# Optimization experiments

Measured on AMD Instinct MI355X. Metric: run time of the kernel, lower is better.

The kernel has to match this reference:

```python
import jax, jax.numpy as jnp
import numpy as np

N_E = 100000       # entities
N_R = 1000         # relations
N_CLASSES = 20000  # class_index.max() + 1
E = 1000000        # edges (triples)
E_HIDDEN = 256
C_HIDDEN = 128
R_HIDDEN = 128
NEG_SLOPE = 0.01   # F.leaky_relu default


def leaky_relu(x):
    return jnp.where(x >= 0, x, NEG_SLOPE * x)


def segment_softmax(x, idx, num_segments):
    # torch_geometric-style scatter softmax over segments given by idx
    m = jax.ops.segment_max(x, idx, num_segments=num_segments)
    ex = jnp.exp(x - m[idx])
    s = jax.ops.segment_sum(ex, idx, num_segments=num_segments)
    return ex / (s[idx] + 1e-16)


def setup_inputs() -> dict:
    key = jax.random.key(0)
    ks = jax.random.split(key, 20)
    inv_c = 1.0 / np.sqrt(C_HIDDEN)
    inv_r = 1.0 / np.sqrt(R_HIDDEN)
    inv_e = 1.0 / np.sqrt(E_HIDDEN)
    inp = {
        "x_e": jax.random.normal(ks[0], (N_E, E_HIDDEN), jnp.float32),
        "edge_index": jax.random.randint(ks[1], (2, E), 0, N_E),
        "rel": jax.random.randint(ks[2], (E,), 0, N_R),
        "triple_num": jax.random.randint(ks[3], (E,), 0, N_E),
        "r_emb": jax.random.normal(ks[4], (N_R, R_HIDDEN), jnp.float32),
        "class_index": jax.random.randint(ks[5], (E,), 0, N_CLASSES),
        "head_class": jax.random.randint(ks[6], (N_CLASSES,), 0, N_E),
        # attention projection vectors (Linear(c_hidden,1,bias=False) weights)
        "a_h1": jax.random.normal(ks[7], (C_HIDDEN,), jnp.float32) * inv_c,
        "a_h2": jax.random.normal(ks[8], (C_HIDDEN,), jnp.float32) * inv_c,
        "a_h3": jax.random.normal(ks[9], (C_HIDDEN,), jnp.float32) * inv_c,
        "a_h4": jax.random.normal(ks[10], (C_HIDDEN,), jnp.float32) * inv_c,
        "a_t1": jax.random.normal(ks[11], (C_HIDDEN,), jnp.float32) * inv_c,
        "a_t2": jax.random.normal(ks[12], (C_HIDDEN,), jnp.float32) * inv_c,
        "a_t3": jax.random.normal(ks[13], (C_HIDDEN,), jnp.float32) * inv_c,
        "a_r1": jax.random.normal(ks[14], (R_HIDDEN,), jnp.float32) * inv_r,
        "a_r2": jax.random.normal(ks[15], (R_HIDDEN,), jnp.float32) * inv_r,
        "a_c": jax.random.normal(ks[16], (C_HIDDEN,), jnp.float32) * inv_c,
        # entity->class-space projections [e_hidden, c_hidden]
        "w_h": jax.random.normal(ks[17], (E_HIDDEN, C_HIDDEN), jnp.float32) * inv_e,
        "w_t": jax.random.normal(ks[18], (E_HIDDEN, C_HIDDEN), jnp.float32) * inv_e,
        # highway gate Linear(c_hidden, c_hidden)
        "hw_w": jax.random.normal(ks[19], (C_HIDDEN, C_HIDDEN), jnp.float32) * inv_c,
        "hw_b": jnp.zeros((C_HIDDEN,), jnp.float32),
    }
    return inp


def reference(x_e, edge_index, rel, triple_num, r_emb, class_index, head_class,
              a_h1, a_h2, a_h3, a_h4, a_t1, a_t2, a_t3, a_r1, a_r2, a_c,
              w_h, w_t, hw_w, hw_b):
    h_idx = edge_index[0]
    t_idx = edge_index[1]

    x_r_h = jax.nn.relu(x_e @ w_h)   # [N_e, C]
    x_r_t = jax.nn.relu(x_e @ w_t)   # [N_e, C]

    # --- level 1: edge attention over triple_num segments ---
    e1 = ((x_r_h @ a_h1)[h_idx] + (x_r_t @ a_t1)[t_idx]) / 2 + (r_emb @ a_r1)[rel]
    alpha = segment_softmax(leaky_relu(e1), triple_num, N_E)       # [E]

    x_t = x_r_t[t_idx] * alpha[:, None]                            # [E, C]
    norm = jnp.linalg.norm(x_t, axis=1, keepdims=True)
    x_t = x_t / jnp.maximum(norm, 1e-12)                           # F.normalize p=2

    # --- level 2: relation/class attention over class_index segments ---
    e_t = x_t @ a_t2                                               # [E]
    e_h = (x_r_h @ a_h2)[h_idx]
    e_r = (r_emb @ a_r2)[rel]
    e_r = (e_r + ((x_r_h @ a_h3)[h_idx] + (x_t @ a_t3)) / 2) / 2
    beta = segment_softmax(leaky_relu(e_t + e_r + e_h), class_index, N_CLASSES)

    # spmm: A[class_index[i], t_idx[i]] = beta[i];  x_class = A @ x_t
    x_class = jax.ops.segment_sum(beta[:, None] * x_t[t_idx],
                                  class_index, num_segments=N_CLASSES)  # [N_CLASSES, C]

    # --- level 3: class->head-entity attention over head_class segments ---
    e_c = (x_class @ a_c) + (x_r_h @ a_h4)[head_class]             # [N_CLASSES]
    gama = segment_softmax(leaky_relu(e_c), head_class, N_E)
    x_e_h = jax.ops.segment_sum(gama[:, None] * x_class,
                                head_class, num_segments=N_E)      # [N_e, C]

    # highway combine
    gate = jax.nn.sigmoid(x_r_h @ hw_w + hw_b)
    return gate * x_e_h + (1.0 - gate) * x_r_h
```

## Files before the change

kernel.cpp:

```cpp
#include <hip/hip_runtime.h>
#include <hip/hip_bf16.h>

#define LRELU(x) ((x) >= 0.f ? (x) : 0.01f * (x))

typedef __attribute__((ext_vector_type(8))) short short8v;
typedef __attribute__((ext_vector_type(4))) float f32x4;

__device__ inline unsigned fenc(float x) {
    unsigned u = __float_as_uint(x);
    return (u & 0x80000000u) ? ~u : (u | 0x80000000u);
}
__device__ inline float fdec(unsigned e) {
    return __uint_as_float((e & 0x80000000u) ? (e ^ 0x80000000u) : ~e);
}

__device__ inline float wred(float v) {
#pragma unroll
    for (int o = 32; o > 0; o >>= 1) v += __shfl_xor(v, o, 64);
    return v;
}
__device__ inline float wredmax(float v) {
#pragma unroll
    for (int o = 32; o > 0; o >>= 1) v = fmaxf(v, __shfl_xor(v, o, 64));
    return v;
}

__device__ inline unsigned short f2bu(float x) {
    __hip_bfloat16 b = __float2bfloat16(x);
    return *reinterpret_cast<unsigned short*>(&b);
}
__device__ inline float bu2f(unsigned short u) {
    return __uint_as_float((unsigned)u << 16);
}

__device__ inline f32x4 mfma16(short8v a, short8v b, f32x4 c) {
    return __builtin_amdgcn_mfma_f32_16x16x32_bf16(a, b, c, 0, 0, 0);
}

__device__ inline void gload16(const void* g, void* l) {
    __builtin_amdgcn_global_load_lds(
        (const __attribute__((address_space(1))) void*)g,
        (__attribute__((address_space(3))) void*)l, 16, 0, 0);
}

__global__ __launch_bounds__(256) void k_convW(
    const float* __restrict__ wh, const float* __restrict__ wt,
    const float* __restrict__ hww, unsigned short* __restrict__ wtb_hi,
    unsigned short* __restrict__ hwt_hi) {
    int id = blockIdx.x * 256 + threadIdx.x;
    if (id < 256 * 256) {
        int n = id >> 8, k = id & 255;
        float v = (n < 128) ? wh[(size_t)k * 128 + n] : wt[(size_t)k * 128 + (n - 128)];
        wtb_hi[(size_t)n * 256 + k] = f2bu(v);
    } else {
        int id2 = id - 256 * 256;
        if (id2 < 128 * 128) {
            int n = id2 >> 7, k = id2 & 127;
            hwt_hi[(size_t)n * 128 + k] = f2bu(hww[(size_t)k * 128 + n]);
        }
    }
}

__global__ __launch_bounds__(256) void k_rel(const float* __restrict__ remb,
                                             const float* __restrict__ ar2,
                                             float* __restrict__ er2, int NR) {
    int lane = threadIdx.x & 63;
    int r = blockIdx.x * 4 + (threadIdx.x >> 6);
    if (r >= NR) return;
    float v0 = remb[(size_t)r * 128 + lane];
    float v1 = remb[(size_t)r * 128 + 64 + lane];
    float p2 = wred(v0 * ar2[lane] + v1 * ar2[64 + lane]);
    if (lane == 0) er2[r] = p2;
}

template <int EPI>
__device__ __forceinline__ void mm_body(
    const float* __restrict__ Af32, const unsigned short* __restrict__ Ah,
    const unsigned short* __restrict__ Bh,
    unsigned short* __restrict__ oh0, unsigned short* __restrict__ oh1,
    float* __restrict__ o0, const float* __restrict__ bias,
    const float* __restrict__ xeh, int M,
    const float* __restrict__ ah2, const float* __restrict__ ah3,
    const float* __restrict__ ah4, const float* __restrict__ at2,
    const float* __restrict__ at3,
    float* __restrict__ hb, float* __restrict__ eh4o,
    float2* __restrict__ pta, const int* __restrict__ tidxg) {
    constexpr int KD = (EPI == 0) ? 256 : 128;
    constexpr int NSTEP = KD / 32;
    __shared__ unsigned short As_h[2][128 * 32];
    __shared__ unsigned short Bs_h[2][128 * 32];

    int bx = blockIdx.x;
    int half = (EPI == 0) ? (bx & 1) : 0;
    int mblk = (EPI == 0) ? (bx >> 1) : bx;
    int row0 = mblk * 128;
    if (row0 + 128 > M) row0 = M - 128;
    int tid = threadIdx.x, w = tid >> 6, l = tid & 63;
    int lr = l & 15, hi4 = l >> 4;
    int srow = l >> 2, sslot = l & 3;

    int arow0 = tid >> 2, aslot0 = tid & 3;
    int arow1 = (256 + tid) >> 2, aslot1 = tid & 3;
    int agr0 = (aslot0 ^ ((arow0 >> 1) & 3)) * 8;
    int agr1 = (aslot1 ^ ((arow1 >> 1) & 3)) * 8;
    float4 rA[4];

    f32x4 acc[2][8];
#pragma unroll
    for (int i = 0; i < 2; i++)
#pragma unroll
        for (int j = 0; j < 8; j++) acc[i][j] = (f32x4){0.f, 0.f, 0.f, 0.f};

    auto loadA = [&](int s) {
        int k0 = s * 32;
        const float* p0 = Af32 + (size_t)(row0 + arow0) * KD + k0 + agr0;
        const float* p1 = Af32 + (size_t)(row0 + arow1) * KD + k0 + agr1;
        rA[0] = *(const float4*)p0;
        rA[1] = *(const float4*)(p0 + 4);
        rA[2] = *(const float4*)p1;
        rA[3] = *(const float4*)(p1 + 4);
    };
    auto writeA = [&](int b) {
        short8v v0, v1;
        float x0[8] = {rA[0].x, rA[0].y, rA[0].z, rA[0].w,
                       rA[1].x, rA[1].y, rA[1].z, rA[1].w};
        float x1[8] = {rA[2].x, rA[2].y, rA[2].z, rA[2].w,
                       rA[3].x, rA[3].y, rA[3].z, rA[3].w};
#pragma unroll
        for (int j = 0; j < 8; j++) {
            v0[j] = (short)f2bu(x0[j]);
            v1[j] = (short)f2bu(x1[j]);
        }
        *(short8v*)&As_h[b][arow0 * 32 + aslot0 * 8] = v0;
        *(short8v*)&As_h[b][arow1 * 32 + aslot1 * 8] = v1;
    };
    auto stageB = [&](int s, int b) {
        int k0 = s * 32;
        constexpr int NU = (EPI == 0) ? 2 : 4;
#pragma unroll
        for (int i = 0; i < NU; i++) {
            int u = w * NU + i;
            int arr = u >> 3, ld = u & 7;
            int row = ld * 16 + srow;
            int klog = (sslot ^ ((row >> 1) & 3)) * 8;
            const unsigned short* src;
            unsigned short* dst;
            if constexpr (EPI == 0) {
                src = Bh + (size_t)(half * 128 + row) * KD;
                dst = Bs_h[b];
            } else {
                if (arr == 0) { src = Ah + (size_t)(row0 + row) * KD; dst = As_h[b]; }
                else          { src = Bh + (size_t)row * KD;          dst = Bs_h[b]; }
            }
            gload16(src + k0 + klog, dst + ld * 512);
        }
    };

    if constexpr (EPI == 0) {
        loadA(0);
        stageB(0, 0);
        writeA(0);
    } else {
        stageB(0, 0);
    }
    __syncthreads();
    for (int s = 0; s < NSTEP; s++) {
        int b = s & 1;
        if (s + 1 < NSTEP) {
            if constexpr (EPI == 0) loadA(s + 1);
            stageB(s + 1, b ^ 1);
        }

        short8v am_h[2];
#pragma unroll
        for (int mr = 0; mr < 2; mr++) {
            int r = w * 32 + mr * 16 + lr;
            int ko = (hi4 ^ ((r >> 1) & 3)) * 8;
            am_h[mr] = *(const short8v*)&As_h[b][r * 32 + ko];
        }
#pragma unroll
        for (int ncc = 0; ncc < 8; ncc += 4) {
            short8v bn_h[4];
#pragma unroll
            for (int j = 0; j < 4; j++) {
                int n = (ncc + j) * 16 + lr;
                int ko = (hi4 ^ ((n >> 1) & 3)) * 8;
                bn_h[j] = *(const short8v*)&Bs_h[b][n * 32 + ko];
            }
#pragma unroll
            for (int mr = 0; mr < 2; mr++)
#pragma unroll
                for (int j = 0; j < 4; j++)
                    acc[mr][ncc + j] = mfma16(am_h[mr], bn_h[j], acc[mr][ncc + j]);
        }
        if constexpr (EPI == 0) {
            if (s + 1 < NSTEP) writeA(b ^ 1);
        }
        __syncthreads();
    }

    if constexpr (EPI == 0) {
        unsigned short* OH = half ? oh1 : oh0;
        const float* v1 = half ? at2 : ah2;
        const float* v2 = half ? at3 : ah3;
#pragma unroll
        for (int mr = 0; mr < 2; mr++)
#pragma unroll
            for (int rr = 0; rr < 4; rr++) {
                int row = row0 + w * 32 + mr * 16 + hi4 * 4 + rr;
                float d0 = 0.f, d1 = 0.f, d2 = 0.f;
#pragma unroll
                for (int nc = 0; nc < 8; nc++) {
                    float v = fmaxf(acc[mr][nc][rr], 0.f);
                    int col = nc * 16 + lr;
                    d0 = fmaf(v, v1[col], d0);
                    d1 = fmaf(v, v2[col], d1);
                    d2 = half ? fmaf(v, v, d2) : fmaf(v, ah4[col], d2);
                }
#pragma unroll
                for (int o = 1; o <= 8; o <<= 1) {
                    d0 += __shfl_xor(d0, o, 64);
                    d1 += __shfl_xor(d1, o, 64);
                    d2 += __shfl_xor(d2, o, 64);
                }
                float inv = 1.f;
                if (half) inv = 1.f / fmaxf(sqrtf(d2), 1e-12f);
#pragma unroll
                for (int nc = 0; nc < 8; nc++) {
                    float v = fmaxf(acc[mr][nc][rr], 0.f);
                    OH[(size_t)row * 128 + nc * 16 + lr] = f2bu(half ? v * inv : v);
                }
                if (lr == 0) {
                    if (half == 0) {
                        hb[row] = d0 + 0.25f * d1;
                        eh4o[row] = d2;
                    } else {
                        float tav = (d0 + 0.25f * d1) * inv;
                        pta[row] = make_float2(tav, __int_as_float(tidxg[row]));
                    }
                }
            }
    } else {
#pragma unroll
        for (int mr = 0; mr < 2; mr++)
#pragma unroll
            for (int rr = 0; rr < 4; rr++) {
                int row = row0 + w * 32 + mr * 16 + hi4 * 4 + rr;
#pragma unroll
                for (int nc = 0; nc < 8; nc++) {
                    int col = nc * 16 + lr;
                    float a = acc[mr][nc][rr] + bias[col];
                    float g = 1.f / (1.f + expf(-a));
                    size_t o = (size_t)row * 128 + col;
                    float af = bu2f(Ah[o]);
                    o0[o] = g * xeh[o] + (1.f - g) * af;
                }
            }
    }
}

__global__ __launch_bounds__(256) void k_mm_proj(
    const float* Af32, const unsigned short* Bh,
    unsigned short* oh0, unsigned short* oh1, int M,
    const float* ah2, const float* ah3, const float* ah4,
    const float* at2, const float* at3,
    float* hb, float* eh4o, float2* pta, const int* tidxg) {
    mm_body<0>(Af32, nullptr, Bh, oh0, oh1, nullptr, nullptr, nullptr, M,
               ah2, ah3, ah4, at2, at3, hb, eh4o, pta, tidxg);
}

__global__ __launch_bounds__(256) void k_mm_hw(
    const unsigned short* Ah, const unsigned short* Bh,
    float* o0, const float* bias, const float* xeh, int M) {
    mm_body<1>(nullptr, Ah, Bh, nullptr, nullptr, o0, bias, xeh, M,
               nullptr, nullptr, nullptr, nullptr, nullptr,
               nullptr, nullptr, nullptr, nullptr);
}

__global__ __launch_bounds__(256) void k_hist(const int* __restrict__ cidx,
                                              int* __restrict__ cnt, int E) {
    int i = blockIdx.x * 256 + threadIdx.x;
    if (i >= E) return;
    atomicAdd(&cnt[cidx[i]], 1);
}

__global__ __launch_bounds__(1024) void k_scan(const int* __restrict__ cnt,
                                               int* __restrict__ off,
                                               int* __restrict__ cur, int NC) {
    __shared__ int wt[16];
    __shared__ int sbase;
    int tid = threadIdx.x, w = tid >> 6, lane = tid & 63;
    if (tid == 0) sbase = 0;
    __syncthreads();
    for (int c0 = 0; c0 < NC; c0 += 1024) {
        int c = c0 + tid;
        int v = (c < NC) ? cnt[c] : 0;
        int x = v;
#pragma unroll
        for (int o = 1; o < 64; o <<= 1) {
            int t = __shfl_up(x, o, 64);
            if (lane >= o) x += t;
        }
        if (lane == 63) wt[w] = x;
        __syncthreads();
        int pre = 0, tot = 0;
#pragma unroll
        for (int i = 0; i < 16; i++) {
            int t = wt[i];
            tot += t;
            if (i < w) pre += t;
        }
        int excl = sbase + pre + x - v;
        if (c < NC) { off[c] = excl; cur[c] = excl; }
        __syncthreads();
        if (tid == 0) sbase += tot;
        __syncthreads();
    }
}

__global__ __launch_bounds__(256) void k_edgescatter(
    const int* __restrict__ cidx, int* __restrict__ cur,
    const int* __restrict__ hidx, const int* __restrict__ tidx,
    const int* __restrict__ rel, const float2* __restrict__ pta,
    const float* __restrict__ hb, const float* __restrict__ er2,
    float2* __restrict__ e2gs, int E) {
    int i = blockIdx.x * 256 + threadIdx.x;
    if (i >= E) return;
    int pos = atomicAdd(&cur[cidx[i]], 1);
    float2 p = pta[tidx[i]];
    float z2 = p.x + hb[hidx[i]] + 0.5f * er2[rel[i]];
    e2gs[pos] = make_float2(LRELU(z2), p.y);
}

__global__ __launch_bounds__(256) void k_spmm2(
    const int* __restrict__ off, const int* __restrict__ cnt,
    const float2* __restrict__ e2gs, const unsigned* __restrict__ xrtn_b,
    float* __restrict__ xclass, const float* __restrict__ ac,
    const float* __restrict__ eh4, const int* __restrict__ hclass,
    float* __restrict__ zc, unsigned* __restrict__ m3, int NC) {
    int lane = threadIdx.x & 63;
    int c = blockIdx.x * 4 + (threadIdx.x >> 6);
    if (c >= NC) return;
    int n = cnt[c];
    float a0 = 0.f, a1 = 0.f;
    if (n > 0) {
        int base = off[c];
        float m = -3.4e38f, s = 0.f;
        for (int j = lane; j < n; j += 64) {
            float z = e2gs[base + j].x;
            if (z > m) { s = s * __expf(m - z) + 1.f; m = z; }
            else s += __expf(z - m);
        }
        float M = wredmax(m);
        s = wred(s * __expf(m - M));
        float inv = 1.f / (s + 1e-16f);
        for (int j0 = 0; j0 < n; j0 += 64) {
            int lim = n - j0;
            if (lim > 64) lim = 64;
            float wv = 0.f;
            int g = 0;
            if (lane < lim) {
                float2 pg = e2gs[base + j0 + lane];
                wv = __expf(pg.x - M) * inv;
                g = __float_as_int(pg.y);
            }
            int jj = 0;
            for (; jj + 8 <= lim; jj += 8) {
                float w0 = __shfl(wv, jj + 0), w1 = __shfl(wv, jj + 1);
                float w2 = __shfl(wv, jj + 2), w3 = __shfl(wv, jj + 3);
                float w4 = __shfl(wv, jj + 4), w5 = __shfl(wv, jj + 5);
                float w6 = __shfl(wv, jj + 6), w7 = __shfl(wv, jj + 7);
                unsigned u0 = xrtn_b[(size_t)__shfl(g, jj + 0) * 64 + lane];
                unsigned u1 = xrtn_b[(size_t)__shfl(g, jj + 1) * 64 + lane];
                unsigned u2 = xrtn_b[(size_t)__shfl(g, jj + 2) * 64 + lane];
                unsigned u3 = xrtn_b[(size_t)__shfl(g, jj + 3) * 64 + lane];
                unsigned u4 = xrtn_b[(size_t)__shfl(g, jj + 4) * 64 + lane];
                unsigned u5 = xrtn_b[(size_t)__shfl(g, jj + 5) * 64 + lane];
                unsigned u6 = xrtn_b[(size_t)__shfl(g, jj + 6) * 64 + lane];
                unsigned u7 = xrtn_b[(size_t)__shfl(g, jj + 7) * 64 + lane];
                a0 = fmaf(w0, bu2f((unsigned short)(u0 & 0xffff)), a0);
                a1 = fmaf(w0, bu2f((unsigned short)(u0 >> 16)), a1);
                a0 = fmaf(w1, bu2f((unsigned short)(u1 & 0xffff)), a0);
                a1 = fmaf(w1, bu2f((unsigned short)(u1 >> 16)), a1);
                a0 = fmaf(w2, bu2f((unsigned short)(u2 & 0xffff)), a0);
                a1 = fmaf(w2, bu2f((unsigned short)(u2 >> 16)), a1);
                a0 = fmaf(w3, bu2f((unsigned short)(u3 & 0xffff)), a0);
                a1 = fmaf(w3, bu2f((unsigned short)(u3 >> 16)), a1);
                a0 = fmaf(w4, bu2f((unsigned short)(u4 & 0xffff)), a0);
                a1 = fmaf(w4, bu2f((unsigned short)(u4 >> 16)), a1);
                a0 = fmaf(w5, bu2f((unsigned short)(u5 & 0xffff)), a0);
                a1 = fmaf(w5, bu2f((unsigned short)(u5 >> 16)), a1);
                a0 = fmaf(w6, bu2f((unsigned short)(u6 & 0xffff)), a0);
                a1 = fmaf(w6, bu2f((unsigned short)(u6 >> 16)), a1);
                a0 = fmaf(w7, bu2f((unsigned short)(u7 & 0xffff)), a0);
                a1 = fmaf(w7, bu2f((unsigned short)(u7 >> 16)), a1);
            }
            for (; jj < lim; jj++) {
                float wj = __shfl(wv, jj);
                unsigned u = xrtn_b[(size_t)__shfl(g, jj) * 64 + lane];
                a0 = fmaf(wj, bu2f((unsigned short)(u & 0xffff)), a0);
                a1 = fmaf(wj, bu2f((unsigned short)(u >> 16)), a1);
            }
        }
    }
    *(float2*)&xclass[(size_t)c * 128 + 2 * lane] = make_float2(a0, a1);
    float p = wred(a0 * ac[2 * lane] + a1 * ac[2 * lane + 1]);
    if (lane == 0) {
        int hc = hclass[c];
        float z = LRELU(p + eh4[hc]);
        zc[c] = z;
        atomicMax(&m3[hc], fenc(z));
    }
}

__global__ __launch_bounds__(256) void k_class2(const int* __restrict__ hclass,
                                                float* __restrict__ zc,
                                                const unsigned* __restrict__ m3,
                                                float* __restrict__ s3, int NC) {
    int c = blockIdx.x * 256 + threadIdx.x;
    if (c >= NC) return;
    int hc = hclass[c];
    float ex = expf(zc[c] - fdec(m3[hc]));
    zc[c] = ex;
    atomicAdd(&s3[hc], ex);
}

__global__ __launch_bounds__(256) void k_class3(
    const int* __restrict__ hclass, const float* __restrict__ zc,
    const float* __restrict__ s3, const float* __restrict__ xclass,
    float* __restrict__ xeh, int NC) {
    int lane = threadIdx.x & 63;
    int c = blockIdx.x * 4 + (threadIdx.x >> 6);
    if (c >= NC) return;
    int hc = hclass[c];
    float gama = zc[c] / (s3[hc] + 1e-16f);
    float v0 = xclass[(size_t)c * 128 + lane], v1 = xclass[(size_t)c * 128 + 64 + lane];
    atomicAdd(&xeh[(size_t)hc * 128 + lane], gama * v0);
    atomicAdd(&xeh[(size_t)hc * 128 + 64 + lane], gama * v1);
}

extern "C" void kernel_launch(void* const* d_in, const int* in_sizes, int n_in,
                              void* d_out, int out_size, void* d_ws, size_t ws_size,
                              hipStream_t stream) {
    (void)n_in; (void)out_size; (void)ws_size;
    const float* xe   = (const float*)d_in[0];
    const int*   eidx = (const int*)d_in[1];
    const int*   rel  = (const int*)d_in[2];
    const float* remb = (const float*)d_in[4];
    const int*   cidx = (const int*)d_in[5];
    const int*   hcls = (const int*)d_in[6];
    const float* ah2  = (const float*)d_in[8];
    const float* ah3  = (const float*)d_in[9];
    const float* ah4  = (const float*)d_in[10];
    const float* at2  = (const float*)d_in[12];
    const float* at3  = (const float*)d_in[13];
    const float* ar2  = (const float*)d_in[15];
    const float* ac   = (const float*)d_in[16];
    const float* wh   = (const float*)d_in[17];
    const float* wt   = (const float*)d_in[18];
    const float* hww  = (const float*)d_in[19];
    const float* hwb  = (const float*)d_in[20];
    float* out = (float*)d_out;

    const int NE = in_sizes[0] / 256;
    const int E  = in_sizes[2];
    const int NR = in_sizes[4] / 128;
    const int NC = in_sizes[6];
    const int* hidx = eidx;
    const int* tidx = eidx + E;

    char* base = (char*)d_ws;
    size_t off0 = 0;
    auto alloc = [&](size_t bytes) -> char* {
        char* r = base + off0;
        off0 = (off0 + bytes + 255) & ~(size_t)255;
        return r;
    };
    float* hb   = (float*)alloc((size_t)NE * 4);
    float* eh4b = (float*)alloc((size_t)NE * 4);
    float2* pta = (float2*)alloc((size_t)NE * 8);
    float* er2b = (float*)alloc((size_t)NR * 4);
    float2* e2gs = (float2*)alloc((size_t)E * 8);
    float* zc   = (float*)alloc((size_t)NC * 4);
    unsigned short* wtb_hi = (unsigned short*)alloc((size_t)256 * 256 * 2);
    unsigned short* hwt_hi = (unsigned short*)alloc((size_t)128 * 128 * 2);
    unsigned short* xrh_hi = (unsigned short*)alloc((size_t)NE * 128 * 2);
    unsigned short* xrtn   = (unsigned short*)alloc((size_t)NE * 128 * 2);
    int* offb = (int*)alloc((size_t)NC * 4);
    int* curb = (int*)alloc((size_t)NC * 4);
    float* xclass = (float*)alloc((size_t)NC * 128 * 4);
    size_t zoff = off0;
    unsigned* m3 = (unsigned*)alloc((size_t)NE * 4);
    float* s3    = (float*)alloc((size_t)NE * 4);
    int* cntb    = (int*)alloc((size_t)NC * 4);
    float* xeh   = (float*)alloc((size_t)NE * 128 * 4);
    size_t zbytes = off0 - zoff;

    hipMemsetAsync(base + zoff, 0, zbytes, stream);

    k_convW<<<(256 * 256 + 128 * 128 + 255) / 256, 256, 0, stream>>>(
        wh, wt, hww, wtb_hi, hwt_hi);
    k_rel<<<(NR + 3) / 4, 256, 0, stream>>>(remb, ar2, er2b, NR);

    k_mm_proj<<<((NE + 127) / 128) * 2, 256, 0, stream>>>(
        xe, wtb_hi, xrh_hi, xrtn, NE,
        ah2, ah3, ah4, at2, at3, hb, eh4b, pta, tidx);

    k_hist<<<(E + 255) / 256, 256, 0, stream>>>(cidx, cntb, E);
    k_scan<<<1, 1024, 0, stream>>>(cntb, offb, curb, NC);

    k_edgescatter<<<(E + 255) / 256, 256, 0, stream>>>(
        cidx, curb, hidx, tidx, rel, pta, hb, er2b, e2gs, E);

    k_spmm2<<<(NC + 3) / 4, 256, 0, stream>>>(offb, cntb, e2gs,
                                              (const unsigned*)xrtn, xclass,
                                              ac, eh4b, hcls, zc, m3, NC);
    k_class2<<<(NC + 255) / 256, 256, 0, stream>>>(hcls, zc, m3, s3, NC);
    k_class3<<<(NC + 3) / 4, 256, 0, stream>>>(hcls, zc, s3, xclass, xeh, NC);

    k_mm_hw<<<(NE + 127) / 128, 256, 0, stream>>>(
        xrh_hi, hwt_hi, out, hwb, xeh, NE);
}
```

Baseline: 282.3 us.

## Stage fp32 A tiles via async LDS loads and skip zeroing of untouched xeh rows

```diff
diff --git a/kernel.cpp b/kernel.cpp
--- a/kernel.cpp
+++ b/kernel.cpp
@@ -79,7 +79,7 @@
     const unsigned short* __restrict__ Bh,
     unsigned short* __restrict__ oh0, unsigned short* __restrict__ oh1,
     float* __restrict__ o0, const float* __restrict__ bias,
-    const float* __restrict__ xeh, int M,
+    const float* __restrict__ xeh, const unsigned* __restrict__ m3f, int M,
     const float* __restrict__ ah2, const float* __restrict__ ah3,
     const float* __restrict__ ah4, const float* __restrict__ at2,
     const float* __restrict__ at3,
@@ -87,7 +87,8 @@
     float2* __restrict__ pta, const int* __restrict__ tidxg) {
     constexpr int KD = (EPI == 0) ? 256 : 128;
     constexpr int NSTEP = KD / 32;
-    __shared__ unsigned short As_h[2][128 * 32];
+    __shared__ float As_f[(EPI == 0) ? 2 : 1][(EPI == 0) ? 128 * 32 : 16];
+    __shared__ unsigned short As_h[(EPI == 1) ? 2 : 1][(EPI == 1) ? 128 * 32 : 16];
     __shared__ unsigned short Bs_h[2][128 * 32];
 
     int bx = blockIdx.x;
@@ -98,12 +99,7 @@
     int tid = threadIdx.x, w = tid >> 6, l = tid & 63;
     int lr = l & 15, hi4 = l >> 4;
     int srow = l >> 2, sslot = l & 3;
-
-    int arow0 = tid >> 2, aslot0 = tid & 3;
-    int arow1 = (256 + tid) >> 2, aslot1 = tid & 3;
-    int agr0 = (aslot0 ^ ((arow0 >> 1) & 3)) * 8;
-    int agr1 = (aslot1 ^ ((arow1 >> 1) & 3)) * 8;
-    float4 rA[4];
+    int arow = l >> 3, afi = l & 7;
 
     f32x4 acc[2][8];
 #pragma unroll
@@ -111,72 +107,63 @@
 #pragma unroll
         for (int j = 0; j < 8; j++) acc[i][j] = (f32x4){0.f, 0.f, 0.f, 0.f};
 
-    auto loadA = [&](int s) {
+    auto stage = [&](int s, int b) {
         int k0 = s * 32;
-        const float* p0 = Af32 + (size_t)(row0 + arow0) * KD + k0 + agr0;
-        const float* p1 = Af32 + (size_t)(row0 + arow1) * KD + k0 + agr1;
-        rA[0] = *(const float4*)p0;
-        rA[1] = *(const float4*)(p0 + 4);
-        rA[2] = *(const float4*)p1;
-        rA[3] = *(const float4*)(p1 + 4);
-    };
-    auto writeA = [&](int b) {
-        short8v v0, v1;
-        float x0[8] = {rA[0].x, rA[0].y, rA[0].z, rA[0].w,
-                       rA[1].x, rA[1].y, rA[1].z, rA[1].w};
-        float x1[8] = {rA[2].x, rA[2].y, rA[2].z, rA[2].w,
-                       rA[3].x, rA[3].y, rA[3].z, rA[3].w};
-#pragma unroll
-        for (int j = 0; j < 8; j++) {
-            v0[j] = (short)f2bu(x0[j]);
-            v1[j] = (short)f2bu(x1[j]);
-        }
-        *(short8v*)&As_h[b][arow0 * 32 + aslot0 * 8] = v0;
-        *(short8v*)&As_h[b][arow1 * 32 + aslot1 * 8] = v1;
-    };
-    auto stageB = [&](int s, int b) {
-        int k0 = s * 32;
-        constexpr int NU = (EPI == 0) ? 2 : 4;
+        constexpr int NU = (EPI == 0) ? 6 : 4;
 #pragma unroll
         for (int i = 0; i < NU; i++) {
             int u = w * NU + i;
-            int arr = u >> 3, ld = u & 7;
-            int row = ld * 16 + srow;
-            int klog = (sslot ^ ((row >> 1) & 3)) * 8;
-            const unsigned short* src;
-            unsigned short* dst;
             if constexpr (EPI == 0) {
-                src = Bh + (size_t)(half * 128 + row) * KD;
-                dst = Bs_h[b];
+                if (u < 16) {
+                    int row = u * 8 + arow;
+                    int gi = afi >> 1, hf = afi & 1;
+                    int sf = ((gi ^ ((row >> 1) & 3)) << 3) + (hf << 2);
+                    gload16(Af32 + (size_t)(row0 + row) * KD + k0 + sf,
+                            (char*)&As_f[b][0] + u * 1024);
+                } else {
+                    int ub = u - 16;
+                    int row = ub * 16 + srow;
+                    int klog = (sslot ^ ((row >> 1) & 3)) * 8;
+                    gload16(Bh + (size_t)(half * 128 + row) * KD + k0 + klog,
+                            (char*)&Bs_h[b][0] + ub * 1024);
+                }
             } else {
-                if (arr == 0) { src = Ah + (size_t)(row0 + row) * KD; dst = As_h[b]; }
-                else          { src = Bh + (size_t)row * KD;          dst = Bs_h[b]; }
-            }
-            gload16(src + k0 + klog, dst + ld * 512);
+                int arr = u >> 3, ld = u & 7;
+                int row = ld * 16 + srow;
+                int klog = (sslot ^ ((row >> 1) & 3)) * 8;
+                if (arr == 0)
+                    gload16(Ah + (size_t)(row0 + row) * KD + k0 + klog,
+                            (char*)&As_h[b][0] + ld * 1024);
+                else
+                    gload16(Bh + (size_t)row * KD + k0 + klog,
+                            (char*)&Bs_h[b][0] + ld * 1024);
+            }
         }
     };
 
-    if constexpr (EPI == 0) {
-        loadA(0);
-        stageB(0, 0);
-        writeA(0);
-    } else {
-        stageB(0, 0);
-    }
+    stage(0, 0);
     __syncthreads();
     for (int s = 0; s < NSTEP; s++) {
         int b = s & 1;
-        if (s + 1 < NSTEP) {
-            if constexpr (EPI == 0) loadA(s + 1);
-            stageB(s + 1, b ^ 1);
-        }
+        if (s + 1 < NSTEP) stage(s + 1, b ^ 1);
 
         short8v am_h[2];
 #pragma unroll
         for (int mr = 0; mr < 2; mr++) {
             int r = w * 32 + mr * 16 + lr;
             int ko = (hi4 ^ ((r >> 1) & 3)) * 8;
-            am_h[mr] = *(const short8v*)&As_h[b][r * 32 + ko];
+            if constexpr (EPI == 0) {
+                float4 f0 = *(const float4*)&As_f[b][r * 32 + ko];
+                float4 f1 = *(const float4*)&As_f[b][r * 32 + ko + 4];
+                short8v v;
+                v[0] = (short)f2bu(f0.x); v[1] = (short)f2bu(f0.y);
+                v[2] = (short)f2bu(f0.z); v[3] = (short)f2bu(f0.w);
+                v[4] = (short)f2bu(f1.x); v[5] = (short)f2bu(f1.y);
+                v[6] = (short)f2bu(f1.z); v[7] = (short)f2bu(f1.w);
+                am_h[mr] = v;
+            } else {
+                am_h[mr] = *(const short8v*)&As_h[b][r * 32 + ko];
+            }
         }
 #pragma unroll
         for (int ncc = 0; ncc < 8; ncc += 4) {
@@ -192,9 +179,6 @@
 #pragma unroll
                 for (int j = 0; j < 4; j++)
                     acc[mr][ncc + j] = mfma16(am_h[mr], bn_h[j], acc[mr][ncc + j]);
-        }
-        if constexpr (EPI == 0) {
-            if (s + 1 < NSTEP) writeA(b ^ 1);
         }
         __syncthreads();
     }
@@ -246,6 +230,7 @@
 #pragma unroll
             for (int rr = 0; rr < 4; rr++) {
                 int row = row0 + w * 32 + mr * 16 + hi4 * 4 + rr;
+                bool touched = (m3f[row] != 0u);
 #pragma unroll
                 for (int nc = 0; nc < 8; nc++) {
                     int col = nc * 16 + lr;
@@ -253,7 +238,9 @@
                     float g = 1.f / (1.f + expf(-a));
                     size_t o = (size_t)row * 128 + col;
                     float af = bu2f(Ah[o]);
-                    o0[o] = g * xeh[o] + (1.f - g) * af;
+                    float xv = 0.f;
+                    if (touched) xv = xeh[o];
+                    o0[o] = g * xv + (1.f - g) * af;
                 }
             }
     }
@@ -265,14 +252,14 @@
     const float* ah2, const float* ah3, const float* ah4,
     const float* at2, const float* at3,
     float* hb, float* eh4o, float2* pta, const int* tidxg) {
-    mm_body<0>(Af32, nullptr, Bh, oh0, oh1, nullptr, nullptr, nullptr, M,
-               ah2, ah3, ah4, at2, at3, hb, eh4o, pta, tidxg);
+    mm_body<0>(Af32, nullptr, Bh, oh0, oh1, nullptr, nullptr, nullptr, nullptr,
+               M, ah2, ah3, ah4, at2, at3, hb, eh4o, pta, tidxg);
 }
 
 __global__ __launch_bounds__(256) void k_mm_hw(
     const unsigned short* Ah, const unsigned short* Bh,
-    float* o0, const float* bias, const float* xeh, int M) {
-    mm_body<1>(nullptr, Ah, Bh, nullptr, nullptr, o0, bias, xeh, M,
+    float* o0, const float* bias, const float* xeh, const unsigned* m3f, int M) {
+    mm_body<1>(nullptr, Ah, Bh, nullptr, nullptr, o0, bias, xeh, m3f, M,
                nullptr, nullptr, nullptr, nullptr, nullptr,
                nullptr, nullptr, nullptr, nullptr);
 }
@@ -413,16 +400,20 @@
     }
 }
 
-__global__ __launch_bounds__(256) void k_class2(const int* __restrict__ hclass,
-                                                float* __restrict__ zc,
-                                                const unsigned* __restrict__ m3,
-                                                float* __restrict__ s3, int NC) {
-    int c = blockIdx.x * 256 + threadIdx.x;
+__global__ __launch_bounds__(256) void k_class2(
+    const int* __restrict__ hclass, float* __restrict__ zc,
+    const unsigned* __restrict__ m3, float* __restrict__ s3,
+    float* __restrict__ xeh, int NC) {
+    int lane = threadIdx.x & 63;
+    int c = blockIdx.x * 4 + (threadIdx.x >> 6);
     if (c >= NC) return;
     int hc = hclass[c];
-    float ex = expf(zc[c] - fdec(m3[hc]));
-    zc[c] = ex;
-    atomicAdd(&s3[hc], ex);
+    *(float2*)&xeh[(size_t)hc * 128 + 2 * lane] = make_float2(0.f, 0.f);
+    if (lane == 0) {
+        float ex = expf(zc[c] - fdec(m3[hc]));
+        zc[c] = ex;
+        atomicAdd(&s3[hc], ex);
+    }
 }
 
 __global__ __launch_bounds__(256) void k_class3(
@@ -489,11 +480,11 @@
     int* offb = (int*)alloc((size_t)NC * 4);
     int* curb = (int*)alloc((size_t)NC * 4);
     float* xclass = (float*)alloc((size_t)NC * 128 * 4);
+    float* xeh    = (float*)alloc((size_t)NE * 128 * 4);
     size_t zoff = off0;
     unsigned* m3 = (unsigned*)alloc((size_t)NE * 4);
     float* s3    = (float*)alloc((size_t)NE * 4);
     int* cntb    = (int*)alloc((size_t)NC * 4);
-    float* xeh   = (float*)alloc((size_t)NE * 128 * 4);
     size_t zbytes = off0 - zoff;
 
     hipMemsetAsync(base + zoff, 0, zbytes, stream);
@@ -515,9 +506,9 @@
     k_spmm2<<<(NC + 3) / 4, 256, 0, stream>>>(offb, cntb, e2gs,
                                               (const unsigned*)xrtn, xclass,
                                               ac, eh4b, hcls, zc, m3, NC);
-    k_class2<<<(NC + 255) / 256, 256, 0, stream>>>(hcls, zc, m3, s3, NC);
+    k_class2<<<(NC + 3) / 4, 256, 0, stream>>>(hcls, zc, m3, s3, xeh, NC);
     k_class3<<<(NC + 3) / 4, 256, 0, stream>>>(hcls, zc, s3, xclass, xeh, NC);
 
     k_mm_hw<<<(NE + 127) / 128, 256, 0, stream>>>(
-        xrh_hi, hwt_hi, out, hwb, xeh, NE);
-}
+        xrh_hi, hwt_hi, out, hwb, xeh, m3, NE);
+}
```

After: 289.5 us. +2.5%, slower.
